# Performance work log

Measured on AMD Instinct MI355X. Metric: run time of the kernel, lower is better.

## Reference

```python
import jax, jax.numpy as jnp
import numpy as np

E = 800_000      # number of edges
D = 256          # d_model_edge
N = 50_000       # number of atoms/nodes


def setup_inputs() -> dict:
    key = jax.random.key(0)
    k1, k2, k3, k4, k5 = jax.random.split(key, 5)
    forces = jax.random.normal(k1, (E, D), dtype=jnp.float32)
    V_st = jax.random.normal(k2, (E, 3), dtype=jnp.float32)
    # MLP([D, D, 1]): Linear(D,D) + act + Linear(D,1). Scaled init for stability.
    W1 = jax.random.normal(k3, (D, D), dtype=jnp.float32) * (1.0 / np.sqrt(D))
    b1 = jnp.zeros((D,), dtype=jnp.float32)
    W2 = jax.random.normal(k4, (D, 1), dtype=jnp.float32) * (1.0 / np.sqrt(D))
    b2 = jnp.zeros((1,), dtype=jnp.float32)
    idx_t = jax.random.randint(k5, (E,), 0, N, dtype=jnp.int64 if jax.config.jax_enable_x64 else jnp.int32)
    return {
        "forces": forces,
        "V_st": V_st,
        "W1": W1,
        "b1": b1,
        "W2": W2,
        "b2": b2,
        "idx_t": idx_t,
        "n_atoms": N,
    }


def reference(forces, V_st, W1, b1, W2, b2, idx_t, n_atoms):
    # out_mlp: Linear(D,D) -> SiLU -> Linear(D,1)
    h = jax.nn.silu(forces @ W1 + b1)          # [E, D]
    s = h @ W2 + b2                            # [E, 1] per-edge scalar
    ev = s * V_st                              # [E, 3] scaled direction vectors
    # scatter-sum over target node indices (reduction='sum')
    out = jax.ops.segment_sum(ev, idx_t, num_segments=n_atoms)  # [N, 3]
    return out
```

## Files before the change

kernel.cpp:

```cpp
#include <hip/hip_runtime.h>
#include <hip/hip_bf16.h>

typedef __attribute__((ext_vector_type(8))) short short8;
typedef __attribute__((ext_vector_type(4))) float floatx4;
typedef unsigned short u16;

#define D 256
#define BM 64
#define NT 256

__device__ __forceinline__ short f2bf(float f) {
    return __builtin_bit_cast(short, __float2bfloat16(f));
}

__global__ void prep_kernel(const float* __restrict__ W1, u16* __restrict__ W1F,
                            float* __restrict__ out, int outn) {
    const int b = blockIdx.x;
    if (b < D) {
        const int k = b, n = threadIdx.x;
        const int k0t = k >> 5, g = (k >> 3) & 3, j = k & 7;
        const int nt = n >> 4, l15 = n & 15;
        W1F[(long)((((k0t << 4) + nt) << 6) + (g << 4) + l15) * 8 + j] = (u16)f2bf(W1[k * D + n]);
    } else {
        int i = (b - D) * 256 + threadIdx.x;
        const int stride = (gridDim.x - D) * 256;
        for (; i < outn; i += stride) out[i] = 0.f;
    }
}

struct R8 { floatx4 f0, f1; };

__launch_bounds__(NT, 4)
__global__ void head_kernel(const float* __restrict__ forces,
                            const float* __restrict__ V_st,
                            const u16*   __restrict__ W1F,
                            const float* __restrict__ b1,
                            const float* __restrict__ W2,
                            const float* __restrict__ b2,
                            const int*   __restrict__ idx_t,
                            float* __restrict__ out,
                            int E) {
    __shared__ u16 Albs[32 * 512];
    __shared__ float s_red[4][BM];

    const int tid  = threadIdx.x;
    const int lane = tid & 63;
    const int wq   = tid >> 6;
    const int l15  = lane & 15;
    const int g    = lane >> 4;

    const long row0 = (long)blockIdx.x * BM;

    float vx = 0.f, vy = 0.f, vz = 0.f;
    int node = -1;
    if (tid < BM) {
        long e = row0 + tid;
        vx = V_st[e * 3 + 0]; vy = V_st[e * 3 + 1]; vz = V_st[e * 3 + 2];
        node = idx_t[e];
    }

    const int arow = tid >> 2;
    const int agg  = tid & 3;
    const float* abase = forces + (row0 + arow) * D + agg * 8;

    R8 r[8];
#pragma unroll
    for (int k0t = 0; k0t < 8; ++k0t) {
        r[k0t].f0 = *(const floatx4*)(abase + k0t * 32);
        r[k0t].f1 = *(const floatx4*)(abase + k0t * 32 + 4);
    }
    const int aslot = ((agg << 4) | (arow & 15)) * 8;
    const int art   = arow >> 4;
#pragma unroll
    for (int k0t = 0; k0t < 8; ++k0t) {
        short8 a;
#pragma unroll
        for (int j = 0; j < 4; ++j) { a[j] = f2bf(r[k0t].f0[j]); a[4 + j] = f2bf(r[k0t].f1[j]); }
        *(short8*)&Albs[(k0t * 4 + art) * 512 + aslot] = a;
    }
    __syncthreads();

    floatx4 acc[4][4];
#pragma unroll
    for (int rt = 0; rt < 4; ++rt)
#pragma unroll
        for (int nc = 0; nc < 4; ++nc)
            acc[rt][nc] = (floatx4){0.f, 0.f, 0.f, 0.f};

#pragma unroll
    for (int k0t = 0; k0t < 8; ++k0t) {
        short8 bf[4], af[4];
#pragma unroll
        for (int nc = 0; nc < 4; ++nc)
            bf[nc] = *(const short8*)(W1F + (long)((k0t * 16 + wq * 4 + nc) * 64 + lane) * 8);
#pragma unroll
        for (int rt = 0; rt < 4; ++rt)
            af[rt] = *(const short8*)&Albs[(k0t * 4 + rt) * 512 + lane * 8];
#pragma unroll
        for (int rt = 0; rt < 4; ++rt)
#pragma unroll
            for (int nc = 0; nc < 4; ++nc)
                acc[rt][nc] = __builtin_amdgcn_mfma_f32_16x16x32_bf16(
                    af[rt], bf[nc], acc[rt][nc], 0, 0, 0);
    }

    float b1v[4], w2v[4];
#pragma unroll
    for (int nc = 0; nc < 4; ++nc) {
        int n = wq * 64 + nc * 16 + l15;
        b1v[nc] = b1[n];
        w2v[nc] = W2[n];
    }
    float part[4][4];
#pragma unroll
    for (int rt = 0; rt < 4; ++rt)
#pragma unroll
        for (int rr = 0; rr < 4; ++rr) {
            float sv = 0.f;
#pragma unroll
            for (int nc = 0; nc < 4; ++nc) {
                float z = acc[rt][nc][rr] + b1v[nc];
                float h = z / (1.f + __expf(-z));
                sv += h * w2v[nc];
            }
            part[rt][rr] = sv;
        }

#pragma unroll
    for (int off = 1; off < 16; off <<= 1)
#pragma unroll
        for (int rt = 0; rt < 4; ++rt)
#pragma unroll
            for (int rr = 0; rr < 4; ++rr)
                part[rt][rr] += __shfl_xor(part[rt][rr], off, 16);

    if (l15 == 0) {
#pragma unroll
        for (int rt = 0; rt < 4; ++rt)
#pragma unroll
            for (int rr = 0; rr < 4; ++rr)
                s_red[wq][rt * 16 + g * 4 + rr] = part[rt][rr];
    }
    __syncthreads();

    if (node >= 0) {
        float sv = s_red[0][tid] + s_red[1][tid] + s_red[2][tid] + s_red[3][tid] + b2[0];
        atomicAdd(&out[(long)node * 3 + 0], sv * vx);
        atomicAdd(&out[(long)node * 3 + 1], sv * vy);
        atomicAdd(&out[(long)node * 3 + 2], sv * vz);
    }
}

extern "C" void kernel_launch(void* const* d_in, const int* in_sizes, int n_in,
                              void* d_out, int out_size, void* d_ws, size_t ws_size,
                              hipStream_t stream) {
    const float* forces = (const float*)d_in[0];
    const float* V_st   = (const float*)d_in[1];
    const float* W1     = (const float*)d_in[2];
    const float* b1     = (const float*)d_in[3];
    const float* W2     = (const float*)d_in[4];
    const float* b2     = (const float*)d_in[5];
    const int*   idx    = (const int*)d_in[6];
    const int E = in_sizes[6];

    u16* W1F = (u16*)d_ws;

    prep_kernel<<<D + 128, 256, 0, stream>>>(W1, W1F, (float*)d_out, out_size);
    const int grid = E / BM;
    head_kernel<<<grid, NT, 0, stream>>>(forces, V_st, W1F, b1, W2, b2, idx,
                                         (float*)d_out, E);
}
```

Measured before the change: 280.4 us.

## Use persistent blocks with W1 fragments held in registers across tiles

```diff
diff --git a/kernel.cpp b/kernel.cpp
--- a/kernel.cpp
+++ b/kernel.cpp
@@ -8,6 +8,7 @@
 #define D 256
 #define BM 64
 #define NT 256
+#define NBLK 512
 
 __device__ __forceinline__ short f2bf(float f) {
     return __builtin_bit_cast(short, __float2bfloat16(f));
@@ -30,7 +31,7 @@
 
 struct R8 { floatx4 f0, f1; };
 
-__launch_bounds__(NT, 4)
+__launch_bounds__(NT, 2)
 __global__ void head_kernel(const float* __restrict__ forces,
                             const float* __restrict__ V_st,
                             const u16*   __restrict__ W1F,
@@ -48,61 +49,15 @@
     const int wq   = tid >> 6;
     const int l15  = lane & 15;
     const int g    = lane >> 4;
+    const int ntiles = E / BM;
 
-    const long row0 = (long)blockIdx.x * BM;
-
-    float vx = 0.f, vy = 0.f, vz = 0.f;
-    int node = -1;
-    if (tid < BM) {
-        long e = row0 + tid;
-        vx = V_st[e * 3 + 0]; vy = V_st[e * 3 + 1]; vz = V_st[e * 3 + 2];
-        node = idx_t[e];
-    }
-
-    const int arow = tid >> 2;
-    const int agg  = tid & 3;
-    const float* abase = forces + (row0 + arow) * D + agg * 8;
-
-    R8 r[8];
+    short8 bfr[32];
 #pragma unroll
-    for (int k0t = 0; k0t < 8; ++k0t) {
-        r[k0t].f0 = *(const floatx4*)(abase + k0t * 32);
-        r[k0t].f1 = *(const floatx4*)(abase + k0t * 32 + 4);
-    }
-    const int aslot = ((agg << 4) | (arow & 15)) * 8;
-    const int art   = arow >> 4;
-#pragma unroll
-    for (int k0t = 0; k0t < 8; ++k0t) {
-        short8 a;
-#pragma unroll
-        for (int j = 0; j < 4; ++j) { a[j] = f2bf(r[k0t].f0[j]); a[4 + j] = f2bf(r[k0t].f1[j]); }
-        *(short8*)&Albs[(k0t * 4 + art) * 512 + aslot] = a;
-    }
-    __syncthreads();
-
-    floatx4 acc[4][4];
-#pragma unroll
-    for (int rt = 0; rt < 4; ++rt)
+    for (int k0t = 0; k0t < 8; ++k0t)
 #pragma unroll
         for (int nc = 0; nc < 4; ++nc)
-            acc[rt][nc] = (floatx4){0.f, 0.f, 0.f, 0.f};
-
-#pragma unroll
-    for (int k0t = 0; k0t < 8; ++k0t) {
-        short8 bf[4], af[4];
-#pragma unroll
-        for (int nc = 0; nc < 4; ++nc)
-            bf[nc] = *(const short8*)(W1F + (long)((k0t * 16 + wq * 4 + nc) * 64 + lane) * 8);
-#pragma unroll
-        for (int rt = 0; rt < 4; ++rt)
-            af[rt] = *(const short8*)&Albs[(k0t * 4 + rt) * 512 + lane * 8];
-#pragma unroll
-        for (int rt = 0; rt < 4; ++rt)
-#pragma unroll
-            for (int nc = 0; nc < 4; ++nc)
-                acc[rt][nc] = __builtin_amdgcn_mfma_f32_16x16x32_bf16(
-                    af[rt], bf[nc], acc[rt][nc], 0, 0, 0);
-    }
+            bfr[k0t * 4 + nc] =
+                *(const short8*)(W1F + (long)((k0t * 16 + wq * 4 + nc) * 64 + lane) * 8);
 
     float b1v[4], w2v[4];
 #pragma unroll
@@ -111,43 +66,100 @@
         b1v[nc] = b1[n];
         w2v[nc] = W2[n];
     }
-    float part[4][4];
-#pragma unroll
-    for (int rt = 0; rt < 4; ++rt)
-#pragma unroll
-        for (int rr = 0; rr < 4; ++rr) {
-            float sv = 0.f;
-#pragma unroll
-            for (int nc = 0; nc < 4; ++nc) {
-                float z = acc[rt][nc][rr] + b1v[nc];
-                float h = z / (1.f + __expf(-z));
-                sv += h * w2v[nc];
-            }
-            part[rt][rr] = sv;
+    const float b2v = b2[0];
+
+    const int arow = tid >> 2;
+    const int agg  = tid & 3;
+    const int aslot = ((agg << 4) | (arow & 15)) * 8;
+    const int art   = arow >> 4;
+
+    for (long t = blockIdx.x; t < (long)ntiles; t += NBLK) {
+        const long row0 = t * BM;
+
+        float vx = 0.f, vy = 0.f, vz = 0.f;
+        int nd = -1;
+        if (lane < 16) {
+            long e = row0 + wq * 16 + lane;
+            vx = V_st[e * 3 + 0]; vy = V_st[e * 3 + 1]; vz = V_st[e * 3 + 2];
+            nd = idx_t[e];
         }
 
+        const float* abase = forces + (row0 + arow) * (long)D + agg * 8;
+        R8 r[8];
 #pragma unroll
-    for (int off = 1; off < 16; off <<= 1)
+        for (int k0t = 0; k0t < 8; ++k0t) {
+            r[k0t].f0 = *(const floatx4*)(abase + k0t * 32);
+            r[k0t].f1 = *(const floatx4*)(abase + k0t * 32 + 4);
+        }
+#pragma unroll
+        for (int k0t = 0; k0t < 8; ++k0t) {
+            short8 a;
+#pragma unroll
+            for (int j = 0; j < 4; ++j) { a[j] = f2bf(r[k0t].f0[j]); a[4 + j] = f2bf(r[k0t].f1[j]); }
+            *(short8*)&Albs[(k0t * 4 + art) * 512 + aslot] = a;
+        }
+        __syncthreads();
+
+        floatx4 acc[4][4];
 #pragma unroll
         for (int rt = 0; rt < 4; ++rt)
 #pragma unroll
-            for (int rr = 0; rr < 4; ++rr)
-                part[rt][rr] += __shfl_xor(part[rt][rr], off, 16);
+            for (int nc = 0; nc < 4; ++nc)
+                acc[rt][nc] = (floatx4){0.f, 0.f, 0.f, 0.f};
 
-    if (l15 == 0) {
+#pragma unroll
+        for (int k0t = 0; k0t < 8; ++k0t) {
+            short8 af[4];
+#pragma unroll
+            for (int rt = 0; rt < 4; ++rt)
+                af[rt] = *(const short8*)&Albs[(k0t * 4 + rt) * 512 + lane * 8];
+#pragma unroll
+            for (int rt = 0; rt < 4; ++rt)
+#pragma unroll
+                for (int nc = 0; nc < 4; ++nc)
+                    acc[rt][nc] = __builtin_amdgcn_mfma_f32_16x16x32_bf16(
+                        af[rt], bfr[k0t * 4 + nc], acc[rt][nc], 0, 0, 0);
+        }
+
+        float part[4][4];
 #pragma unroll
         for (int rt = 0; rt < 4; ++rt)
 #pragma unroll
-            for (int rr = 0; rr < 4; ++rr)
-                s_red[wq][rt * 16 + g * 4 + rr] = part[rt][rr];
-    }
-    __syncthreads();
+            for (int rr = 0; rr < 4; ++rr) {
+                float sv = 0.f;
+#pragma unroll
+                for (int nc = 0; nc < 4; ++nc) {
+                    float z = acc[rt][nc][rr] + b1v[nc];
+                    float h = z / (1.f + __expf(-z));
+                    sv += h * w2v[nc];
+                }
+                part[rt][rr] = sv;
+            }
 
-    if (node >= 0) {
-        float sv = s_red[0][tid] + s_red[1][tid] + s_red[2][tid] + s_red[3][tid] + b2[0];
-        atomicAdd(&out[(long)node * 3 + 0], sv * vx);
-        atomicAdd(&out[(long)node * 3 + 1], sv * vy);
-        atomicAdd(&out[(long)node * 3 + 2], sv * vz);
+#pragma unroll
+        for (int off = 1; off < 16; off <<= 1)
+#pragma unroll
+            for (int rt = 0; rt < 4; ++rt)
+#pragma unroll
+                for (int rr = 0; rr < 4; ++rr)
+                    part[rt][rr] += __shfl_xor(part[rt][rr], off, 16);
+
+        if (l15 == 0) {
+#pragma unroll
+            for (int rt = 0; rt < 4; ++rt)
+#pragma unroll
+                for (int rr = 0; rr < 4; ++rr)
+                    s_red[wq][rt * 16 + g * 4 + rr] = part[rt][rr];
+        }
+        __syncthreads();
+
+        if (nd >= 0) {
+            int row = wq * 16 + lane;
+            float sv = s_red[0][row] + s_red[1][row] + s_red[2][row] + s_red[3][row] + b2v;
+            atomicAdd(&out[(long)nd * 3 + 0], sv * vx);
+            atomicAdd(&out[(long)nd * 3 + 1], sv * vy);
+            atomicAdd(&out[(long)nd * 3 + 2], sv * vz);
+        }
     }
 }
 
@@ -166,7 +178,6 @@
     u16* W1F = (u16*)d_ws;
 
     prep_kernel<<<D + 128, 256, 0, stream>>>(W1, W1F, (float*)d_out, out_size);
-    const int grid = E / BM;
-    head_kernel<<<grid, NT, 0, stream>>>(forces, V_st, W1F, b1, W2, b2, idx,
+    head_kernel<<<NBLK, NT, 0, stream>>>(forces, V_st, W1F, b1, W2, b2, idx,
                                          (float*)d_out, E);
 }
```

New measurement: 295.6 us. +5.4%, slower.

## Split per-edge scatter out of GEMM head kernel into a separate atomic pass

Applied to the files above, without the earlier changes.

```diff
diff --git a/kernel.cpp b/kernel.cpp
--- a/kernel.cpp
+++ b/kernel.cpp
@@ -30,6 +30,7 @@
 
 struct R8 { floatx4 f0, f1; };
 
+template<bool SCATTER>
 __launch_bounds__(NT, 4)
 __global__ void head_kernel(const float* __restrict__ forces,
                             const float* __restrict__ V_st,
@@ -39,6 +40,7 @@
                             const float* __restrict__ b2,
                             const int*   __restrict__ idx_t,
                             float* __restrict__ out,
+                            float* __restrict__ s_out,
                             int E) {
     __shared__ u16 Albs[32 * 512];
     __shared__ float s_red[4][BM];
@@ -53,7 +55,7 @@
 
     float vx = 0.f, vy = 0.f, vz = 0.f;
     int node = -1;
-    if (tid < BM) {
+    if (SCATTER && tid < BM) {
         long e = row0 + tid;
         vx = V_st[e * 3 + 0]; vy = V_st[e * 3 + 1]; vz = V_st[e * 3 + 2];
         node = idx_t[e];
@@ -61,8 +63,7 @@
 
     const int arow = tid >> 2;
     const int agg  = tid & 3;
-    const float* abase = forces + (row0 + arow) * D + agg * 8;
-
+    const float* abase = forces + (row0 + arow) * (long)D + agg * 8;
     R8 r[8];
 #pragma unroll
     for (int k0t = 0; k0t < 8; ++k0t) {
@@ -125,7 +126,6 @@
             }
             part[rt][rr] = sv;
         }
-
 #pragma unroll
     for (int off = 1; off < 16; off <<= 1)
 #pragma unroll
@@ -143,11 +143,33 @@
     }
     __syncthreads();
 
-    if (node >= 0) {
+    if (tid < BM) {
         float sv = s_red[0][tid] + s_red[1][tid] + s_red[2][tid] + s_red[3][tid] + b2[0];
-        atomicAdd(&out[(long)node * 3 + 0], sv * vx);
-        atomicAdd(&out[(long)node * 3 + 1], sv * vy);
-        atomicAdd(&out[(long)node * 3 + 2], sv * vz);
+        if (SCATTER) {
+            if (node >= 0) {
+                atomicAdd(&out[(long)node * 3 + 0], sv * vx);
+                atomicAdd(&out[(long)node * 3 + 1], sv * vy);
+                atomicAdd(&out[(long)node * 3 + 2], sv * vz);
+            }
+        } else {
+            s_out[row0 + tid] = sv;
+        }
+    }
+}
+
+__global__ void scatter_kernel(const float* __restrict__ s,
+                               const float* __restrict__ V_st,
+                               const int* __restrict__ idx_t,
+                               float* __restrict__ out, int E) {
+    const int stride = gridDim.x * blockDim.x;
+    for (int e = blockIdx.x * blockDim.x + threadIdx.x; e < E; e += stride) {
+        float sv = s[e];
+        long b = (long)e * 3;
+        float vx = V_st[b], vy = V_st[b + 1], vz = V_st[b + 2];
+        long nd = (long)idx_t[e];
+        atomicAdd(&out[nd * 3 + 0], sv * vx);
+        atomicAdd(&out[nd * 3 + 1], sv * vy);
+        atomicAdd(&out[nd * 3 + 2], sv * vz);
     }
 }
 
@@ -164,9 +186,16 @@
     const int E = in_sizes[6];
 
     u16* W1F = (u16*)d_ws;
+    float* s = (float*)((char*)d_ws + 131072);
 
     prep_kernel<<<D + 128, 256, 0, stream>>>(W1, W1F, (float*)d_out, out_size);
     const int grid = E / BM;
-    head_kernel<<<grid, NT, 0, stream>>>(forces, V_st, W1F, b1, W2, b2, idx,
-                                         (float*)d_out, E);
-}
+    if (ws_size >= 131072 + (size_t)E * 4) {
+        head_kernel<false><<<grid, NT, 0, stream>>>(forces, V_st, W1F, b1, W2, b2,
+                                                    idx, (float*)d_out, s, E);
+        scatter_kernel<<<2048, 256, 0, stream>>>(s, V_st, idx, (float*)d_out, E);
+    } else {
+        head_kernel<true><<<grid, NT, 0, stream>>>(forces, V_st, W1F, b1, W2, b2,
+                                                   idx, (float*)d_out, s, E);
+    }
+}
```

After: 349.0 us. 24.5% more time.

## Process four row tiles per block with double-buffered LDS software pipeline

Applied to the files above, without the earlier changes.

```diff
diff --git a/kernel.cpp b/kernel.cpp
--- a/kernel.cpp
+++ b/kernel.cpp
@@ -7,6 +7,7 @@
 
 #define D 256
 #define BM 64
+#define TILES 4
 #define NT 256
 
 __device__ __forceinline__ short f2bf(float f) {
@@ -30,7 +31,7 @@
 
 struct R8 { floatx4 f0, f1; };
 
-__launch_bounds__(NT, 4)
+__launch_bounds__(NT, 2)
 __global__ void head_kernel(const float* __restrict__ forces,
                             const float* __restrict__ V_st,
                             const u16*   __restrict__ W1F,
@@ -40,8 +41,8 @@
                             const int*   __restrict__ idx_t,
                             float* __restrict__ out,
                             int E) {
-    __shared__ u16 Albs[32 * 512];
-    __shared__ float s_red[4][BM];
+    __shared__ u16 Albs[2][32 * 512];
+    __shared__ float s_red[TILES][4][BM];
 
     const int tid  = threadIdx.x;
     const int lane = tid & 63;
@@ -49,60 +50,13 @@
     const int l15  = lane & 15;
     const int g    = lane >> 4;
 
-    const long row0 = (long)blockIdx.x * BM;
+    const long blk0 = (long)blockIdx.x * (BM * TILES);
 
-    float vx = 0.f, vy = 0.f, vz = 0.f;
-    int node = -1;
-    if (tid < BM) {
-        long e = row0 + tid;
-        vx = V_st[e * 3 + 0]; vy = V_st[e * 3 + 1]; vz = V_st[e * 3 + 2];
-        node = idx_t[e];
-    }
-
-    const int arow = tid >> 2;
-    const int agg  = tid & 3;
-    const float* abase = forces + (row0 + arow) * D + agg * 8;
-
-    R8 r[8];
-#pragma unroll
-    for (int k0t = 0; k0t < 8; ++k0t) {
-        r[k0t].f0 = *(const floatx4*)(abase + k0t * 32);
-        r[k0t].f1 = *(const floatx4*)(abase + k0t * 32 + 4);
-    }
-    const int aslot = ((agg << 4) | (arow & 15)) * 8;
-    const int art   = arow >> 4;
-#pragma unroll
-    for (int k0t = 0; k0t < 8; ++k0t) {
-        short8 a;
-#pragma unroll
-        for (int j = 0; j < 4; ++j) { a[j] = f2bf(r[k0t].f0[j]); a[4 + j] = f2bf(r[k0t].f1[j]); }
-        *(short8*)&Albs[(k0t * 4 + art) * 512 + aslot] = a;
-    }
-    __syncthreads();
-
-    floatx4 acc[4][4];
-#pragma unroll
-    for (int rt = 0; rt < 4; ++rt)
-#pragma unroll
-        for (int nc = 0; nc < 4; ++nc)
-            acc[rt][nc] = (floatx4){0.f, 0.f, 0.f, 0.f};
-
-#pragma unroll
-    for (int k0t = 0; k0t < 8; ++k0t) {
-        short8 bf[4], af[4];
-#pragma unroll
-        for (int nc = 0; nc < 4; ++nc)
-            bf[nc] = *(const short8*)(W1F + (long)((k0t * 16 + wq * 4 + nc) * 64 + lane) * 8);
-#pragma unroll
-        for (int rt = 0; rt < 4; ++rt)
-            af[rt] = *(const short8*)&Albs[(k0t * 4 + rt) * 512 + lane * 8];
-#pragma unroll
-        for (int rt = 0; rt < 4; ++rt)
-#pragma unroll
-            for (int nc = 0; nc < 4; ++nc)
-                acc[rt][nc] = __builtin_amdgcn_mfma_f32_16x16x32_bf16(
-                    af[rt], bf[nc], acc[rt][nc], 0, 0, 0);
-    }
+    const long my_e = blk0 + tid;
+    const float mvx = V_st[my_e * 3 + 0];
+    const float mvy = V_st[my_e * 3 + 1];
+    const float mvz = V_st[my_e * 3 + 2];
+    const int  mnd  = idx_t[my_e];
 
     float b1v[4], w2v[4];
 #pragma unroll
@@ -111,43 +65,110 @@
         b1v[nc] = b1[n];
         w2v[nc] = W2[n];
     }
-    float part[4][4];
+    const float b2v = b2[0];
+
+    const int arow  = tid >> 2;
+    const int agg   = tid & 3;
+    const int aslot = ((agg << 4) | (arow & 15)) * 8;
+    const int art   = arow >> 4;
+
+    auto BURST = [&](int t, R8* r) {
+        const float* abase = forces + (blk0 + t * BM + arow) * (long)D + agg * 8;
 #pragma unroll
-    for (int rt = 0; rt < 4; ++rt)
+        for (int k0t = 0; k0t < 8; ++k0t) {
+            r[k0t].f0 = *(const floatx4*)(abase + k0t * 32);
+            r[k0t].f1 = *(const floatx4*)(abase + k0t * 32 + 4);
+        }
+    };
+    auto CVTW = [&](int buf, const R8* r) {
 #pragma unroll
-        for (int rr = 0; rr < 4; ++rr) {
-            float sv = 0.f;
+        for (int k0t = 0; k0t < 8; ++k0t) {
+            short8 a;
 #pragma unroll
-            for (int nc = 0; nc < 4; ++nc) {
-                float z = acc[rt][nc][rr] + b1v[nc];
-                float h = z / (1.f + __expf(-z));
-                sv += h * w2v[nc];
-            }
-            part[rt][rr] = sv;
+            for (int j = 0; j < 4; ++j) { a[j] = f2bf(r[k0t].f0[j]); a[4 + j] = f2bf(r[k0t].f1[j]); }
+            *(short8*)&Albs[buf][(k0t * 4 + art) * 512 + aslot] = a;
         }
-
-#pragma unroll
-    for (int off = 1; off < 16; off <<= 1)
+    };
+    auto COMPUTE = [&](int buf, int t) {
+        floatx4 acc[4][4];
 #pragma unroll
         for (int rt = 0; rt < 4; ++rt)
 #pragma unroll
-            for (int rr = 0; rr < 4; ++rr)
-                part[rt][rr] += __shfl_xor(part[rt][rr], off, 16);
-
-    if (l15 == 0) {
+            for (int nc = 0; nc < 4; ++nc)
+                acc[rt][nc] = (floatx4){0.f, 0.f, 0.f, 0.f};
+#pragma unroll
+        for (int k0t = 0; k0t < 8; ++k0t) {
+            short8 bf[4], af[4];
+#pragma unroll
+            for (int nc = 0; nc < 4; ++nc)
+                bf[nc] = *(const short8*)(W1F + (long)((k0t * 16 + wq * 4 + nc) * 64 + lane) * 8);
+#pragma unroll
+            for (int rt = 0; rt < 4; ++rt)
+                af[rt] = *(const short8*)&Albs[buf][(k0t * 4 + rt) * 512 + lane * 8];
+#pragma unroll
+            for (int rt = 0; rt < 4; ++rt)
+#pragma unroll
+                for (int nc = 0; nc < 4; ++nc)
+                    acc[rt][nc] = __builtin_amdgcn_mfma_f32_16x16x32_bf16(
+                        af[rt], bf[nc], acc[rt][nc], 0, 0, 0);
+        }
+        float part[4][4];
 #pragma unroll
         for (int rt = 0; rt < 4; ++rt)
 #pragma unroll
-            for (int rr = 0; rr < 4; ++rr)
-                s_red[wq][rt * 16 + g * 4 + rr] = part[rt][rr];
+            for (int rr = 0; rr < 4; ++rr) {
+                float sv = 0.f;
+#pragma unroll
+                for (int nc = 0; nc < 4; ++nc) {
+                    float z = acc[rt][nc][rr] + b1v[nc];
+                    float h = z / (1.f + __expf(-z));
+                    sv += h * w2v[nc];
+                }
+                part[rt][rr] = sv;
+            }
+#pragma unroll
+        for (int off = 1; off < 16; off <<= 1)
+#pragma unroll
+            for (int rt = 0; rt < 4; ++rt)
+#pragma unroll
+                for (int rr = 0; rr < 4; ++rr)
+                    part[rt][rr] += __shfl_xor(part[rt][rr], off, 16);
+        if (l15 == 0) {
+#pragma unroll
+            for (int rt = 0; rt < 4; ++rt)
+#pragma unroll
+                for (int rr = 0; rr < 4; ++rr)
+                    s_red[t][wq][rt * 16 + g * 4 + rr] = part[rt][rr];
+        }
+    };
+
+    {
+        R8 r[8];
+        BURST(0, r);
+        CVTW(0, r);
     }
     __syncthreads();
 
-    if (node >= 0) {
-        float sv = s_red[0][tid] + s_red[1][tid] + s_red[2][tid] + s_red[3][tid] + b2[0];
-        atomicAdd(&out[(long)node * 3 + 0], sv * vx);
-        atomicAdd(&out[(long)node * 3 + 1], sv * vy);
-        atomicAdd(&out[(long)node * 3 + 2], sv * vz);
+#pragma unroll
+    for (int t = 1; t < TILES; ++t) {
+        R8 r[8];
+        BURST(t, r);
+        __builtin_amdgcn_sched_barrier(0);
+        COMPUTE((t - 1) & 1, t - 1);
+        CVTW(t & 1, r);
+        __syncthreads();
+    }
+
+    COMPUTE((TILES - 1) & 1, TILES - 1);
+    __syncthreads();
+
+    {
+        const int tt = tid >> 6, row = tid & 63;
+        float sv = s_red[tt][0][row] + s_red[tt][1][row]
+                 + s_red[tt][2][row] + s_red[tt][3][row] + b2v;
+        atomicAdd(&out[(long)mnd * 3 + 0], sv * mvx);
+        atomicAdd(&out[(long)mnd * 3 + 1], sv * mvy);
+        atomicAdd(&out[(long)mnd * 3 + 2], sv * mvz);
     }
 }
 
@@ -166,7 +187,7 @@
     u16* W1F = (u16*)d_ws;
 
     prep_kernel<<<D + 128, 256, 0, stream>>>(W1, W1F, (float*)d_out, out_size);
-    const int grid = E / BM;
+    const int grid = E / (BM * TILES);
     head_kernel<<<grid, NT, 0, stream>>>(forces, V_st, W1F, b1, W2, b2, idx,
                                          (float*)d_out, E);
 }
```

After: 422.9 us. 1.51x slower.
